# Performance work log

Measured on AMD Instinct MI355X. Metric: run time of the kernel, lower is better.

## Reference

```python
import math
import jax, jax.numpy as jnp
import numpy as np

EMB = 1024
HEADS = 16
EXPAND = 2
HEAD_D = EMB // HEADS * EXPAND  # 128
N, S = 2, 2048


def setup_inputs() -> dict:
    key = jax.random.key(0)
    ks = jax.random.split(key, 10)
    lim = 1.0 / math.sqrt(EMB)  # nn.Linear default init range
    inp = {
        "query": jax.random.normal(ks[0], (N, S, EMB), dtype=jnp.float32),
        "key": jax.random.normal(ks[1], (N, S, EMB), dtype=jnp.float32),
        "value": jax.random.normal(ks[2], (N, S, EMB), dtype=jnp.float32),
        "mask": jax.random.randint(ks[3], (1, S, S), 0, 2, dtype=jnp.int32),
        "Wq": jax.random.uniform(ks[4], (EMB * EXPAND, EMB), jnp.float32, -lim, lim),
        "bq": jax.random.uniform(ks[5], (EMB * EXPAND,), jnp.float32, -lim, lim),
        "Wk": jax.random.uniform(ks[6], (EMB * EXPAND, EMB), jnp.float32, -lim, lim),
        "bk": jax.random.uniform(ks[7], (EMB * EXPAND,), jnp.float32, -lim, lim),
        "Wv": jax.random.uniform(ks[8], (EMB * EXPAND, EMB), jnp.float32, -lim, lim),
        "bv": jax.random.uniform(ks[9], (EMB * EXPAND,), jnp.float32, -lim, lim),
    }
    return inp


def _split_heads(x):
    # (N, S, H*D) -> (N, H, S, D)
    n, s, _ = x.shape
    return x.reshape(n, s, HEADS, HEAD_D).transpose(0, 2, 1, 3)


def reference(query, key, value, mask, Wq, bq, Wk, bk, Wv, bv):
    Q = _split_heads(jax.nn.relu(query @ Wq.T + bq))  # (N,H,S,D)
    K = _split_heads(jax.nn.relu(key @ Wk.T + bk))
    V = _split_heads(jax.nn.relu(value @ Wv.T + bv))
    scale = 1.0 / math.sqrt(HEAD_D)
    scores = jnp.einsum("nhqd,nhkd->nhqk", Q, K) * scale  # (N,H,S,S)
    scores = jnp.where(mask[None, :, :, :] == 0, jnp.float32(-1e7), scores)
    probs = jax.nn.softmax(scores, axis=-1)
    y = jnp.einsum("nhqk,nhkd->nhqd", probs, V)  # (N,H,S,D)
    return y.transpose(0, 2, 1, 3).reshape(query.shape[0], S, HEADS * HEAD_D)
```

## Files before the change

### kernel.cpp

```cpp
#include <hip/hip_runtime.h>

typedef __bf16 bf16;
typedef __bf16 bf16x8 __attribute__((ext_vector_type(8)));
typedef __bf16 bf16x4 __attribute__((ext_vector_type(4)));
typedef float f32x4 __attribute__((ext_vector_type(4)));

#define MFMA_BF16(A, B, C) __builtin_amdgcn_mfma_f32_16x16x32_bf16((A), (B), (C), 0, 0, 0)

#define EMB 1024
#define ODIM 2048
#define SEQ 2048
#define HEADS 16
#define HD 128

__device__ __forceinline__ void gload16(const bf16* g, const bf16* l) {
  __builtin_amdgcn_global_load_lds(
      (const __attribute__((address_space(1))) unsigned int*)(const void*)g,
      (__attribute__((address_space(3))) unsigned int*)(void*)l, 16, 0, 0);
}

__global__ __launch_bounds__(256) void cvt_bf16_k(const float* __restrict__ q,
                                                  const float* __restrict__ k,
                                                  const float* __restrict__ v,
                                                  const float* __restrict__ Wq,
                                                  const float* __restrict__ Wk,
                                                  const float* __restrict__ Wv,
                                                  bf16* __restrict__ Xall,
                                                  bf16* __restrict__ Wall) {
  const unsigned XV = 4096u * 1024u / 8u;
  const unsigned WV = 2048u * 1024u / 8u;
  unsigned id = blockIdx.x * 256 + threadIdx.x;
  const float* src;
  bf16* dst;
  size_t off;
  if (id < 3 * XV) {
    unsigned p = id / XV;
    off = (size_t)(id - p * XV) * 8;
    src = (p == 0) ? q : (p == 1 ? k : v);
    dst = Xall + (size_t)p * (4096u * 1024u);
  } else {
    unsigned id2 = id - 3 * XV;
    unsigned p = id2 / WV;
    off = (size_t)(id2 - p * WV) * 8;
    src = (p == 0) ? Wq : (p == 1 ? Wk : Wv);
    dst = Wall + (size_t)p * (2048u * 1024u);
  }
  float4 a = *(const float4*)(src + off);
  float4 b = *(const float4*)(src + off + 4);
  bf16x8 o;
  o[0] = (bf16)a.x; o[1] = (bf16)a.y; o[2] = (bf16)a.z; o[3] = (bf16)a.w;
  o[4] = (bf16)b.x; o[5] = (bf16)b.y; o[6] = (bf16)b.z; o[7] = (bf16)b.w;
  *(bf16x8*)(dst + off) = o;
}

__global__ __launch_bounds__(256) void build_maskbits_k(const int* __restrict__ mask,
                                                        unsigned long long* __restrict__ mb) {
  int w = blockIdx.x * 256 + threadIdx.x;
  int q = w >> 5, c = w & 31;
  const int4* m4 = reinterpret_cast<const int4*>(mask + (size_t)q * SEQ + c * 64);
  unsigned long long bits = 0ull;
#pragma unroll
  for (int i = 0; i < 16; ++i) {
    int4 v = m4[i];
    if (v.x) bits |= 1ull << (i * 4 + 0);
    if (v.y) bits |= 1ull << (i * 4 + 1);
    if (v.z) bits |= 1ull << (i * 4 + 2);
    if (v.w) bits |= 1ull << (i * 4 + 3);
  }
  mb[w] = bits;
}

__global__ __launch_bounds__(256) void proj_gemm_k(const bf16* __restrict__ Xall,
                                                   const bf16* __restrict__ Wall,
                                                   const float* __restrict__ bq,
                                                   const float* __restrict__ bk_,
                                                   const float* __restrict__ bv_,
                                                   bf16* __restrict__ Qb,
                                                   bf16* __restrict__ Kb,
                                                   bf16* __restrict__ Vt,
                                                   float qscale) {
  __shared__ union {
    struct { bf16 A[128 * 64]; bf16 B[128 * 64]; } s;
    bf16 C[128][136];
  } sm;

  const int t = threadIdx.x;
  const int lane = t & 63;
  const int wid = t >> 6;
  const int wm = wid >> 1, wn = wid & 1;
  const int lr = lane & 15, lg = lane >> 4;
  const int z = blockIdx.z;
  const int m0 = blockIdx.y * 128;
  const int n0 = blockIdx.x * 128;
  const bf16* X = Xall + (size_t)z * (4096u * 1024u);
  const bf16* W = Wall + (size_t)z * (2048u * 1024u);
  const float* bias = (z == 0) ? bq : (z == 1 ? bk_ : bv_);
  const float oscale = (z == 0) ? qscale : 1.0f;

  const int sr_ = t >> 3;
  const int scb = (t & 7) * 16;

  f32x4 acc[4][4];
#pragma unroll
  for (int i = 0; i < 4; ++i)
#pragma unroll
    for (int j = 0; j < 4; ++j) acc[i][j] = {0.f, 0.f, 0.f, 0.f};

  for (int k0 = 0; k0 < EMB; k0 += 64) {
#pragma unroll
    for (int j = 0; j < 4; ++j) {
      int r = j * 32 + sr_;
      int cb = scb ^ ((r & 7) << 4);
      gload16(X + (size_t)(m0 + r) * EMB + k0 + (cb >> 1), &sm.s.A[j * 2048 + t * 8]);
    }
#pragma unroll
    for (int j = 0; j < 4; ++j) {
      int r = j * 32 + sr_;
      int cb = scb ^ ((r & 7) << 4);
      gload16(W + (size_t)(n0 + r) * EMB + k0 + (cb >> 1), &sm.s.B[j * 2048 + t * 8]);
    }
    __syncthreads();

    bf16x8 af[4][2], bfr[4][2];
#pragma unroll
    for (int i = 0; i < 4; ++i)
#pragma unroll
      for (int s = 0; s < 2; ++s) {
        int ra = wm * 64 + i * 16 + lr;
        int ca = (s * 64 + lg * 16) ^ ((ra & 7) << 4);
        af[i][s] = *(const bf16x8*)&sm.s.A[ra * 64 + (ca >> 1)];
        int rb = wn * 64 + i * 16 + lr;
        int cb2 = (s * 64 + lg * 16) ^ ((rb & 7) << 4);
        bfr[i][s] = *(const bf16x8*)&sm.s.B[rb * 64 + (cb2 >> 1)];
      }
#pragma unroll
    for (int s = 0; s < 2; ++s)
#pragma unroll
      for (int mi = 0; mi < 4; ++mi)
#pragma unroll
        for (int ni = 0; ni < 4; ++ni)
          acc[mi][ni] = MFMA_BF16(af[mi][s], bfr[ni][s], acc[mi][ni]);
    __syncthreads();
  }

  float bv4[4];
#pragma unroll
  for (int ni = 0; ni < 4; ++ni) bv4[ni] = bias[n0 + wn * 64 + ni * 16 + lr];

  if (z < 2) {
    bf16* outN = (z == 0) ? Qb : Kb;
#pragma unroll
    for (int mi = 0; mi < 4; ++mi)
#pragma unroll
      for (int ni = 0; ni < 4; ++ni)
#pragma unroll
        for (int j = 0; j < 4; ++j) {
          float v = fmaxf(acc[mi][ni][j] + bv4[ni], 0.f) * oscale;
          int row = m0 + wm * 64 + mi * 16 + lg * 4 + j;
          int col = n0 + wn * 64 + ni * 16 + lr;
          outN[(size_t)row * ODIM + col] = (bf16)v;
        }
  } else {
#pragma unroll
    for (int mi = 0; mi < 4; ++mi)
#pragma unroll
      for (int ni = 0; ni < 4; ++ni)
#pragma unroll
        for (int j = 0; j < 4; ++j) {
          float v = fmaxf(acc[mi][ni][j] + bv4[ni], 0.f);
          int rit = wm * 64 + mi * 16 + lg * 4 + j;
          int cit = wn * 64 + ni * 16 + lr;
          sm.C[cit][rit] = (bf16)v;
        }
    __syncthreads();
    const int n = m0 >> 11;
    const int s0 = m0 & (SEQ - 1);
    const int h = blockIdx.x;
    bf16* base = Vt + ((size_t)(n * HEADS + h) * HD) * SEQ + s0;
#pragma unroll
    for (int i = 0; i < 8; ++i) {
      int cid = i * 256 + t;
      int d = cid >> 4, c = cid & 15;
      *(bf16x8*)(base + (size_t)d * SEQ + c * 8) = *(const bf16x8*)&sm.C[d][c * 8];
    }
  }
}


__device__ __forceinline__ int kswz(int r, int c) {
  int b = (r << 8) | (c << 1);
  b ^= (r & 7) << 4;
  return b >> 1;
}
__device__ __forceinline__ int vswz(int d, int s) {
  int b = (d << 7) | (s << 1);
  b ^= (d & 7) << 4;
  return b >> 1;
}

__global__ __launch_bounds__(512, 2) void attn_k(const bf16* __restrict__ Qb,
                                                 const bf16* __restrict__ Kb,
                                                 const bf16* __restrict__ Vt,
                                                 const unsigned long long* __restrict__ mb,
                                                 float* __restrict__ out) {
  __shared__ bf16 Ks[2][64 * 128];
  __shared__ bf16 Vs[2][128 * 64];
  __shared__ bf16 Ps[8][32][72];

  const int t = threadIdx.x;
  const int lane = t & 63;
  const int w = t >> 6;
  const int lr = lane & 15, lg = lane >> 4;

  const int bid = blockIdx.x;
  const int swz = (bid & 7) * 32 + (bid >> 3);
  const int nh = swz >> 3;
  const int qt = swz & 7;
  const int n = nh >> 4, h = nh & 15;
  const int qrow = qt * 256 + w * 32;

  bf16x8 qf[2][4];
#pragma unroll
  for (int g = 0; g < 2; ++g) {
    const bf16* qp = Qb + (size_t)(n * SEQ + qrow + g * 16 + lr) * ODIM + h * HD + lg * 8;
#pragma unroll
    for (int ks = 0; ks < 4; ++ks) qf[g][ks] = *(const bf16x8*)(qp + ks * 32);
  }

  bf16x8 onesA;
  {
    bf16 o1 = (bf16)((lr == 0) ? 1.0f : 0.0f);
#pragma unroll
    for (int j = 0; j < 8; ++j) onesA[j] = o1;
  }

  const bf16* Kg = Kb + (size_t)(n * SEQ) * ODIM + h * HD;
  const bf16* Vg = Vt + (size_t)nh * HD * SEQ;

  const int rK = t >> 4, cK = t & 15;
  const int dV = t >> 3, cV = t & 7;
  const bf16* kgp = Kg + (size_t)rK * ODIM + cK * 8;
  const bf16* vgp = Vg + (size_t)dV * SEQ + cV * 8;

  bf16x8 kreg[2], vreg[2];
#pragma unroll
  for (int i = 0; i < 2; ++i) kreg[i] = *(const bf16x8*)(kgp + (size_t)i * 32 * ODIM);
#pragma unroll
  for (int i = 0; i < 2; ++i) vreg[i] = *(const bf16x8*)(vgp + (size_t)i * 64 * SEQ);
#pragma unroll
  for (int i = 0; i < 2; ++i) *(bf16x8*)&Ks[0][kswz(rK + i * 32, cK * 8)] = kreg[i];
#pragma unroll
  for (int i = 0; i < 2; ++i) *(bf16x8*)&Vs[0][vswz(dV + i * 64, cV * 8)] = vreg[i];
  __syncthreads();

  f32x4 oacc[2][9];
#pragma unroll
  for (int g = 0; g < 2; ++g)
#pragma unroll
    for (int i = 0; i < 9; ++i) oacc[g][i] = {0.f, 0.f, 0.f, 0.f};
  float mrun[2] = {-3.0e38f, -3.0e38f};

  const int NT = SEQ / 64;
  for (int kt = 0; kt < NT; ++kt) {
    const int cur = kt & 1;

    if (kt + 1 < NT) {
      const bf16* kn = kgp + (size_t)(kt + 1) * 64 * ODIM;
      const bf16* vn = vgp + (size_t)(kt + 1) * 64;
#pragma unroll
      for (int i = 0; i < 2; ++i) kreg[i] = *(const bf16x8*)(kn + (size_t)i * 32 * ODIM);
#pragma unroll
      for (int i = 0; i < 2; ++i) vreg[i] = *(const bf16x8*)(vn + (size_t)i * 64 * SEQ);
    }

    unsigned long long mw0 = mb[(size_t)(qrow + lr) * 32 + kt];
    unsigned long long mw1 = mb[(size_t)(qrow + 16 + lr) * 32 + kt];

    f32x4 sacc[2][4];
#pragma unroll
    for (int f = 0; f < 4; ++f)
#pragma unroll
      for (int j = 0; j < 4; ++j) {
        int kk = f * 16 + lg * 4 + j;
        sacc[0][f][j] = ((mw0 >> kk) & 1ull) ? 0.f : -1.0e7f;
        sacc[1][f][j] = ((mw1 >> kk) & 1ull) ? 0.f : -1.0e7f;
      }
#pragma unroll
    for (int f = 0; f < 4; ++f) {
#pragma unroll
      for (int ks = 0; ks < 4; ++ks) {
        bf16x8 kf = *(const bf16x8*)&Ks[cur][kswz(f * 16 + lr, ks * 32 + lg * 8)];
        sacc[0][f] = MFMA_BF16(kf, qf[0][ks], sacc[0][f]);
        sacc[1][f] = MFMA_BF16(kf, qf[1][ks], sacc[1][f]);
      }
    }

    float mt[2] = {-3.0e38f, -3.0e38f};
#pragma unroll
    for (int g = 0; g < 2; ++g) {
#pragma unroll
      for (int f = 0; f < 4; ++f) {
        float a = fmaxf(sacc[g][f][0], sacc[g][f][1]);
        float b = fmaxf(sacc[g][f][2], sacc[g][f][3]);
        mt[g] = fmaxf(mt[g], fmaxf(a, b));
      }
      mt[g] = fmaxf(mt[g], __shfl_xor(mt[g], 16));
      mt[g] = fmaxf(mt[g], __shfl_xor(mt[g], 32));
    }

    if (!__all((mt[0] <= mrun[0] + 8.0f) && (mt[1] <= mrun[1] + 8.0f))) {
#pragma unroll
      for (int g = 0; g < 2; ++g) {
        float mnew = fmaxf(mrun[g], mt[g]);
        float alpha = exp2f(mrun[g] - mnew);
        mrun[g] = mnew;
#pragma unroll
        for (int df = 0; df < 9; ++df)
#pragma unroll
          for (int j = 0; j < 4; ++j) oacc[g][df][j] *= alpha;
      }
    }

#pragma unroll
    for (int g = 0; g < 2; ++g)
#pragma unroll
      for (int f = 0; f < 4; ++f) {
        bf16x4 pw;
#pragma unroll
        for (int j = 0; j < 4; ++j) pw[j] = (bf16)exp2f(sacc[g][f][j] - mrun[g]);
        *(bf16x4*)&Ps[w][g * 16 + lr][f * 16 + lg * 4] = pw;
      }

    if (kt + 1 < NT) {
#pragma unroll
      for (int i = 0; i < 2; ++i) *(bf16x8*)&Ks[cur ^ 1][kswz(rK + i * 32, cK * 8)] = kreg[i];
#pragma unroll
      for (int i = 0; i < 2; ++i) *(bf16x8*)&Vs[cur ^ 1][vswz(dV + i * 64, cV * 8)] = vreg[i];
    }

    bf16x8 pB[2][2];
#pragma unroll
    for (int g = 0; g < 2; ++g)
#pragma unroll
      for (int ks = 0; ks < 2; ++ks)
        pB[g][ks] = *(const bf16x8*)&Ps[w][g * 16 + lr][ks * 32 + lg * 8];

#pragma unroll
    for (int df = 0; df < 8; ++df) {
#pragma unroll
      for (int ks = 0; ks < 2; ++ks) {
        bf16x8 vf = *(const bf16x8*)&Vs[cur][vswz(df * 16 + lr, ks * 32 + lg * 8)];
        oacc[0][df] = MFMA_BF16(vf, pB[0][ks], oacc[0][df]);
        oacc[1][df] = MFMA_BF16(vf, pB[1][ks], oacc[1][df]);
      }
    }
#pragma unroll
    for (int ks = 0; ks < 2; ++ks) {
      oacc[0][8] = MFMA_BF16(onesA, pB[0][ks], oacc[0][8]);
      oacc[1][8] = MFMA_BF16(onesA, pB[1][ks], oacc[1][8]);
    }
    __syncthreads();
  }

#pragma unroll
  for (int g = 0; g < 2; ++g) {
    float l = __shfl(oacc[g][8][0], lr);
    float inv = 1.0f / l;
    float* obase = out + (size_t)(n * SEQ + qrow + g * 16 + lr) * ODIM + h * HD;
#pragma unroll
    for (int df = 0; df < 8; ++df) {
      f32x4 o;
#pragma unroll
      for (int j = 0; j < 4; ++j) o[j] = oacc[g][df][j] * inv;
      *(f32x4*)(obase + df * 16 + lg * 4) = o;
    }
  }
}

extern "C" void kernel_launch(void* const* d_in, const int* in_sizes, int n_in,
                              void* d_out, int out_size, void* d_ws, size_t ws_size,
                              hipStream_t stream) {
  const float* q   = (const float*)d_in[0];
  const float* k   = (const float*)d_in[1];
  const float* v   = (const float*)d_in[2];
  const int*  mask = (const int*)d_in[3];
  const float* Wq  = (const float*)d_in[4];
  const float* bq  = (const float*)d_in[5];
  const float* Wk  = (const float*)d_in[6];
  const float* bk  = (const float*)d_in[7];
  const float* Wv  = (const float*)d_in[8];
  const float* bv  = (const float*)d_in[9];
  float* out = (float*)d_out;

  char* ws = (char*)d_ws;
  const size_t PLANE = (size_t)4096 * 2048 * sizeof(bf16);
  bf16* Qb = (bf16*)ws;
  bf16* Kb = (bf16*)(ws + PLANE);
  bf16* Vt = (bf16*)(ws + 2 * PLANE);
  unsigned long long* mb = (unsigned long long*)(ws + 3 * PLANE);
  bf16* Xall = (bf16*)(ws + 3 * PLANE + (4u << 20));
  bf16* Wall = (bf16*)(ws + 3 * PLANE + (4u << 20) + (size_t)3 * 4096 * 1024 * 2);

  const float qscale = 0.08838834764831845f * 1.4426950408889634f;

  cvt_bf16_k<<<9216, 256, 0, stream>>>(q, k, v, Wq, Wk, Wv, Xall, Wall);
  build_maskbits_k<<<256, 256, 0, stream>>>(mask, mb);
  proj_gemm_k<<<dim3(16, 32, 3), 256, 0, stream>>>(Xall, Wall, bq, bk, bv, Qb, Kb, Vt, qscale);
  attn_k<<<256, 512, 0, stream>>>(Qb, Kb, Vt, mb, out);
}
```

Before: 198.2 us.

## Software-pipeline attention: overlap next QK with current softmax and previous PV

```diff
diff --git a/kernel.cpp b/kernel.cpp
--- a/kernel.cpp
+++ b/kernel.cpp
@@ -203,13 +203,13 @@
                                                  const bf16* __restrict__ Vt,
                                                  const unsigned long long* __restrict__ mb,
                                                  float* __restrict__ out) {
-  __shared__ bf16 Ks[2][64 * 128];
-  __shared__ bf16 Vs[2][128 * 64];
+  __shared__ bf16 KsB[2][64 * 128];
+  __shared__ bf16 VsB[4][128 * 64];
   __shared__ bf16 Ps[8][32][72];
 
-  const int t = threadIdx.x;
-  const int lane = t & 63;
-  const int w = t >> 6;
+  const int tid = threadIdx.x;
+  const int lane = tid & 63;
+  const int w = tid >> 6;
   const int lr = lane & 15, lg = lane >> 4;
 
   const int bid = blockIdx.x;
@@ -237,22 +237,31 @@
   const bf16* Kg = Kb + (size_t)(n * SEQ) * ODIM + h * HD;
   const bf16* Vg = Vt + (size_t)nh * HD * SEQ;
 
-  const int rK = t >> 4, cK = t & 15;
-  const int dV = t >> 3, cV = t & 7;
+  const int rK = tid >> 4, cK = tid & 15;
+  const int dV = tid >> 3, cV = tid & 7;
   const bf16* kgp = Kg + (size_t)rK * ODIM + cK * 8;
   const bf16* vgp = Vg + (size_t)dV * SEQ + cV * 8;
 
   bf16x8 kreg[2], vreg[2];
-#pragma unroll
-  for (int i = 0; i < 2; ++i) kreg[i] = *(const bf16x8*)(kgp + (size_t)i * 32 * ODIM);
-#pragma unroll
-  for (int i = 0; i < 2; ++i) vreg[i] = *(const bf16x8*)(vgp + (size_t)i * 64 * SEQ);
-#pragma unroll
-  for (int i = 0; i < 2; ++i) *(bf16x8*)&Ks[0][kswz(rK + i * 32, cK * 8)] = kreg[i];
-#pragma unroll
-  for (int i = 0; i < 2; ++i) *(bf16x8*)&Vs[0][vswz(dV + i * 64, cV * 8)] = vreg[i];
-  __syncthreads();
-
+
+  auto issue_loads = [&](int u, bf16x8 (&kr)[2], bf16x8 (&vr)[2]) {
+    const bf16* kn = kgp + (size_t)u * 64 * ODIM;
+    const bf16* vn = vgp + (size_t)u * 64;
+#pragma unroll
+    for (int i = 0; i < 2; ++i) kr[i] = *(const bf16x8*)(kn + (size_t)i * 32 * ODIM);
+#pragma unroll
+    for (int i = 0; i < 2; ++i) vr[i] = *(const bf16x8*)(vn + (size_t)i * 64 * SEQ);
+  };
+  auto write_stage = [&](int u, bf16x8 (&kr)[2], bf16x8 (&vr)[2]) {
+    bf16* Kd = KsB[u & 1];
+    bf16* Vd = VsB[u & 3];
+#pragma unroll
+    for (int i = 0; i < 2; ++i) *(bf16x8*)&Kd[kswz(rK + i * 32, cK * 8)] = kr[i];
+#pragma unroll
+    for (int i = 0; i < 2; ++i) *(bf16x8*)&Vd[vswz(dV + i * 64, cV * 8)] = vr[i];
+  };
+
+  f32x4 saccA[2][4], saccB[2][4];
   f32x4 oacc[2][9];
 #pragma unroll
   for (int g = 0; g < 2; ++g)
@@ -260,96 +269,43 @@
     for (int i = 0; i < 9; ++i) oacc[g][i] = {0.f, 0.f, 0.f, 0.f};
   float mrun[2] = {-3.0e38f, -3.0e38f};
 
-  const int NT = SEQ / 64;
-  for (int kt = 0; kt < NT; ++kt) {
-    const int cur = kt & 1;
-
-    if (kt + 1 < NT) {
-      const bf16* kn = kgp + (size_t)(kt + 1) * 64 * ODIM;
-      const bf16* vn = vgp + (size_t)(kt + 1) * 64;
-#pragma unroll
-      for (int i = 0; i < 2; ++i) kreg[i] = *(const bf16x8*)(kn + (size_t)i * 32 * ODIM);
-#pragma unroll
-      for (int i = 0; i < 2; ++i) vreg[i] = *(const bf16x8*)(vn + (size_t)i * 64 * SEQ);
-    }
-
-    unsigned long long mw0 = mb[(size_t)(qrow + lr) * 32 + kt];
-    unsigned long long mw1 = mb[(size_t)(qrow + 16 + lr) * 32 + kt];
-
-    f32x4 sacc[2][4];
+  auto qk = [&](int u, f32x4 (&sn)[2][4], unsigned long long mw0, unsigned long long mw1) {
+    const bf16* Kst = KsB[u & 1];
 #pragma unroll
     for (int f = 0; f < 4; ++f)
 #pragma unroll
       for (int j = 0; j < 4; ++j) {
         int kk = f * 16 + lg * 4 + j;
-        sacc[0][f][j] = ((mw0 >> kk) & 1ull) ? 0.f : -1.0e7f;
-        sacc[1][f][j] = ((mw1 >> kk) & 1ull) ? 0.f : -1.0e7f;
+        sn[0][f][j] = ((mw0 >> kk) & 1ull) ? 0.f : -1.0e7f;
+        sn[1][f][j] = ((mw1 >> kk) & 1ull) ? 0.f : -1.0e7f;
       }
+    __builtin_amdgcn_s_setprio(1);
 #pragma unroll
     for (int f = 0; f < 4; ++f) {
 #pragma unroll
       for (int ks = 0; ks < 4; ++ks) {
-        bf16x8 kf = *(const bf16x8*)&Ks[cur][kswz(f * 16 + lr, ks * 32 + lg * 8)];
-        sacc[0][f] = MFMA_BF16(kf, qf[0][ks], sacc[0][f]);
-        sacc[1][f] = MFMA_BF16(kf, qf[1][ks], sacc[1][f]);
+        bf16x8 kf = *(const bf16x8*)&Kst[kswz(f * 16 + lr, ks * 32 + lg * 8)];
+        sn[0][f] = MFMA_BF16(kf, qf[0][ks], sn[0][f]);
+        sn[1][f] = MFMA_BF16(kf, qf[1][ks], sn[1][f]);
       }
     }
-
-    float mt[2] = {-3.0e38f, -3.0e38f};
-#pragma unroll
-    for (int g = 0; g < 2; ++g) {
-#pragma unroll
-      for (int f = 0; f < 4; ++f) {
-        float a = fmaxf(sacc[g][f][0], sacc[g][f][1]);
-        float b = fmaxf(sacc[g][f][2], sacc[g][f][3]);
-        mt[g] = fmaxf(mt[g], fmaxf(a, b));
-      }
-      mt[g] = fmaxf(mt[g], __shfl_xor(mt[g], 16));
-      mt[g] = fmaxf(mt[g], __shfl_xor(mt[g], 32));
-    }
-
-    if (!__all((mt[0] <= mrun[0] + 8.0f) && (mt[1] <= mrun[1] + 8.0f))) {
-#pragma unroll
-      for (int g = 0; g < 2; ++g) {
-        float mnew = fmaxf(mrun[g], mt[g]);
-        float alpha = exp2f(mrun[g] - mnew);
-        mrun[g] = mnew;
-#pragma unroll
-        for (int df = 0; df < 9; ++df)
-#pragma unroll
-          for (int j = 0; j < 4; ++j) oacc[g][df][j] *= alpha;
-      }
-    }
-
-#pragma unroll
-    for (int g = 0; g < 2; ++g)
-#pragma unroll
-      for (int f = 0; f < 4; ++f) {
-        bf16x4 pw;
-#pragma unroll
-        for (int j = 0; j < 4; ++j) pw[j] = (bf16)exp2f(sacc[g][f][j] - mrun[g]);
-        *(bf16x4*)&Ps[w][g * 16 + lr][f * 16 + lg * 4] = pw;
-      }
-
-    if (kt + 1 < NT) {
-#pragma unroll
-      for (int i = 0; i < 2; ++i) *(bf16x8*)&Ks[cur ^ 1][kswz(rK + i * 32, cK * 8)] = kreg[i];
-#pragma unroll
-      for (int i = 0; i < 2; ++i) *(bf16x8*)&Vs[cur ^ 1][vswz(dV + i * 64, cV * 8)] = vreg[i];
-    }
-
+    __builtin_amdgcn_s_setprio(0);
+  };
+
+  auto pv = [&](int u) {
     bf16x8 pB[2][2];
 #pragma unroll
     for (int g = 0; g < 2; ++g)
 #pragma unroll
       for (int ks = 0; ks < 2; ++ks)
         pB[g][ks] = *(const bf16x8*)&Ps[w][g * 16 + lr][ks * 32 + lg * 8];
-
+    const bf16* Vst = VsB[u & 3];
+    __builtin_amdgcn_s_setprio(1);
 #pragma unroll
     for (int df = 0; df < 8; ++df) {
 #pragma unroll
       for (int ks = 0; ks < 2; ++ks) {
-        bf16x8 vf = *(const bf16x8*)&Vs[cur][vswz(df * 16 + lr, ks * 32 + lg * 8)];
+        bf16x8 vf = *(const bf16x8*)&Vst[vswz(df * 16 + lr, ks * 32 + lg * 8)];
         oacc[0][df] = MFMA_BF16(vf, pB[0][ks], oacc[0][df]);
         oacc[1][df] = MFMA_BF16(vf, pB[1][ks], oacc[1][df]);
       }
@@ -359,8 +315,88 @@
       oacc[0][8] = MFMA_BF16(onesA, pB[0][ks], oacc[0][8]);
       oacc[1][8] = MFMA_BF16(onesA, pB[1][ks], oacc[1][8]);
     }
+    __builtin_amdgcn_s_setprio(0);
+  };
+
+  const int NT = SEQ / 64;
+
+  {
+    bf16x8 kreg2[2], vreg2[2];
+    issue_loads(0, kreg, vreg);
+    issue_loads(1, kreg2, vreg2);
+    write_stage(0, kreg, vreg);
+    write_stage(1, kreg2, vreg2);
     __syncthreads();
-  }
+    unsigned long long mw0 = mb[(size_t)(qrow + lr) * 32 + 0];
+    unsigned long long mw1 = mb[(size_t)(qrow + 16 + lr) * 32 + 0];
+    qk(0, saccA, mw0, mw1);
+  }
+
+  auto body = [&](int kt, f32x4 (&sc)[2][4], f32x4 (&sn)[2][4]) {
+    unsigned long long mwa = 0ull, mwb = 0ull;
+    if (kt + 1 < NT) {
+      mwa = mb[(size_t)(qrow + lr) * 32 + kt + 1];
+      mwb = mb[(size_t)(qrow + 16 + lr) * 32 + kt + 1];
+    }
+    if (kt + 2 < NT) issue_loads(kt + 2, kreg, vreg);
+    if (kt + 1 < NT) qk(kt + 1, sn, mwa, mwb);
+
+    float mt0 = -3.0e38f, mt1 = -3.0e38f;
+#pragma unroll
+    for (int f = 0; f < 4; ++f) {
+      mt0 = fmaxf(mt0, fmaxf(fmaxf(sc[0][f][0], sc[0][f][1]), fmaxf(sc[0][f][2], sc[0][f][3])));
+      mt1 = fmaxf(mt1, fmaxf(fmaxf(sc[1][f][0], sc[1][f][1]), fmaxf(sc[1][f][2], sc[1][f][3])));
+    }
+    mt0 = fmaxf(mt0, __shfl_xor(mt0, 16));
+    mt0 = fmaxf(mt0, __shfl_xor(mt0, 32));
+    mt1 = fmaxf(mt1, __shfl_xor(mt1, 16));
+    mt1 = fmaxf(mt1, __shfl_xor(mt1, 32));
+
+    float a0 = 1.0f, a1 = 1.0f;
+    bool need = !__all((mt0 <= mrun[0] + 8.0f) && (mt1 <= mrun[1] + 8.0f));
+    if (need) {
+      float m0n = fmaxf(mrun[0], mt0);
+      float m1n = fmaxf(mrun[1], mt1);
+      a0 = exp2f(mrun[0] - m0n);
+      a1 = exp2f(mrun[1] - m1n);
+      mrun[0] = m0n;
+      mrun[1] = m1n;
+    }
+    bf16x4 pk[2][4];
+#pragma unroll
+    for (int g = 0; g < 2; ++g)
+#pragma unroll
+      for (int f = 0; f < 4; ++f)
+#pragma unroll
+        for (int j = 0; j < 4; ++j) pk[g][f][j] = (bf16)exp2f(sc[g][f][j] - mrun[g]);
+
+    if (kt > 0) pv(kt - 1);
+
+    if (need) {
+#pragma unroll
+      for (int df = 0; df < 9; ++df)
+#pragma unroll
+        for (int j = 0; j < 4; ++j) {
+          oacc[0][df][j] *= a0;
+          oacc[1][df][j] *= a1;
+        }
+    }
+
+#pragma unroll
+    for (int g = 0; g < 2; ++g)
+#pragma unroll
+      for (int f = 0; f < 4; ++f)
+        *(bf16x4*)&Ps[w][g * 16 + lr][f * 16 + lg * 4] = pk[g][f];
+
+    if (kt + 2 < NT) write_stage(kt + 2, kreg, vreg);
+    __syncthreads();
+  };
+
+  for (int kt = 0; kt < NT; kt += 2) {
+    body(kt, saccA, saccB);
+    body(kt + 1, saccB, saccA);
+  }
+  pv(NT - 1);
 
 #pragma unroll
   for (int g = 0; g < 2; ++g) {
```

After: 338.6 us. +70.8%, slower.
